# Kernel tuning notes

Measured on AMD Instinct MI355X. Metric: run time of the kernel, lower is better.

## Reference

```python
import jax, jax.numpy as jnp
import numpy as np

NUM_EXECUTORS = 50
NUM_DAG_FEATURES = 3
EMB_DAG = 16
EMB_GLOB = 16
HIDDEN = [64, 64, 32]
B = 60000            # number of jobs (one per env in the batched rollout)
NODES_PER_JOB = 10
NODE_FEAT = 5


def _init_mlp(key, dims):
    ws, bs = [], []
    for i in range(len(dims) - 1):
        key, k = jax.random.split(key)
        scale = 1.0 / np.sqrt(dims[i])
        ws.append(jax.random.uniform(k, (dims[i], dims[i + 1]), jnp.float32, -scale, scale))
        bs.append(jnp.zeros((dims[i + 1],), jnp.float32))
    return ws, bs


def setup_inputs() -> dict:
    rng = np.random.default_rng(0)
    n_nodes = B * NODES_PER_JOB
    # dag_batch.ptr: job i owns nodes [i*NODES_PER_JOB, (i+1)*NODES_PER_JOB)
    ptr = np.arange(B + 1, dtype=np.int64) * NODES_PER_JOB
    job_indices = rng.permutation(B).astype(np.int64)
    # ragged action counts per job (exec_mask is a prefix mask of length num_exec_acts[i])
    num_exec_acts = rng.integers(1, NUM_EXECUTORS + 1, size=B).astype(np.int64)
    n_sel = num_exec_acts[job_indices]
    T = int(n_sel.sum())
    # per-ragged-row executor index: concat([arange(n) for n in n_sel]), vectorized
    starts = np.cumsum(n_sel) - n_sel
    exec_act_idx = (np.arange(T, dtype=np.int64) - np.repeat(starts, n_sel)).astype(np.int64)

    key = jax.random.key(0)
    k_x, k_hd, k_hg, k_mlp = jax.random.split(key, 4)
    x = jax.random.normal(k_x, (n_nodes, NODE_FEAT), jnp.float32)
    h_dag = jax.random.normal(k_hd, (B, EMB_DAG), jnp.float32)
    h_glob = jax.random.normal(k_hg, (B, EMB_GLOB), jnp.float32)

    in_dim = NUM_DAG_FEATURES + EMB_DAG + EMB_GLOB + 1  # 36
    ws, bs = _init_mlp(k_mlp, [in_dim] + HIDDEN + [1])

    return {
        "x": x,
        "h_dag": h_dag,
        "h_glob": h_glob,
        "ptr": jnp.asarray(ptr),
        "job_indices": jnp.asarray(job_indices),
        "num_exec_acts": jnp.asarray(num_exec_acts),
        "exec_act_idx": jnp.asarray(exec_act_idx),
        "W1": ws[0], "b1": bs[0],
        "W2": ws[1], "b2": bs[1],
        "W3": ws[2], "b3": bs[2],
        "W4": ws[3], "b4": bs[3],
    }


def reference(x, h_dag, h_glob, ptr, job_indices, num_exec_acts, exec_act_idx,
              W1, b1, W2, b2, W3, b3, W4, b4):
    T = exec_act_idx.shape[0]                       # total ragged action rows (static)
    J = job_indices.shape[0]
    # masked gather: dag features at each dag's start node, then select jobs
    x_dag = x[ptr[:-1], :NUM_DAG_FEATURES][job_indices]        # [J, 3]
    h_dag_sel = h_dag[job_indices]                              # [J, 16]
    x_h_dag = jnp.concatenate([x_dag, h_dag_sel], axis=1)       # [J, 19]
    # variable repeat_interleave -> gather by repeated row index
    n_sel = num_exec_acts[job_indices]
    rpt = jnp.repeat(jnp.arange(J), n_sel, total_repeat_length=T)
    x_h_rpt = x_h_dag[rpt]                                      # [T, 19]
    h_glob_rpt = h_glob[rpt]                                    # [T, 16]
    # exec action feature: k / num_executors for the k-th valid executor
    exec_actions = (exec_act_idx.astype(x.dtype) / NUM_EXECUTORS)[:, None]  # [T, 1]
    h = jnp.concatenate([x_h_rpt, h_glob_rpt, exec_actions], axis=1)        # [T, 36]
    h = jax.nn.relu(h @ W1 + b1)
    h = jax.nn.relu(h @ W2 + b2)
    h = jax.nn.relu(h @ W3 + b3)
    scores = (h @ W4 + b4).squeeze(-1)                          # [T]
    return scores
```

## Files before the change

### kernel.cpp

```cpp
#include <hip/hip_runtime.h>

#define TPB 256

using half8  = __attribute__((ext_vector_type(8))) _Float16;
using fp16x2 = __attribute__((ext_vector_type(2))) __fp16;
using f32x4  = __attribute__((ext_vector_type(4))) float;

static __device__ __forceinline__ unsigned short h2u(_Float16 h) {
    union { _Float16 h; unsigned short u; } v; v.h = h; return v.u;
}
static __device__ __forceinline__ unsigned pkrtz(float a, float b) {
    fp16x2 h = __builtin_amdgcn_cvt_pkrtz(a, b);
    return __builtin_bit_cast(unsigned, h);
}
template <int CTRL>
static __device__ __forceinline__ float dppmov(float x) {
    return __int_as_float(__builtin_amdgcn_mov_dpp(__float_as_int(x), CTRL, 0xF, 0xF, true));
}
#define DPP_SWAP 0xB1

__global__ __launch_bounds__(TPB) void k_prep(const float* __restrict__ x,
                                              const float* __restrict__ h_dag,
                                              const float* __restrict__ h_glob,
                                              const int* __restrict__ ptr,
                                              const int* __restrict__ job_indices,
                                              const int* __restrict__ num_exec_acts,
                                              int J, unsigned int* __restrict__ feat,
                                              int* __restrict__ bsum)
{
    __shared__ int sc[TPB];
    int j = blockIdx.x * TPB + threadIdx.x;
    int v = 0;
    if (j < J) {
        int ji   = job_indices[j];
        v        = num_exec_acts[ji];
        int node = ptr[ji];
        float f[40];
        f[0] = x[node * 5 + 0];
        f[1] = x[node * 5 + 1];
        f[2] = x[node * 5 + 2];
#pragma unroll
        for (int c = 0; c < 16; c++) f[3 + c]  = h_dag[ji * 16 + c];
#pragma unroll
        for (int c = 0; c < 16; c++) f[19 + c] = h_glob[j * 16 + c];
#pragma unroll
        for (int c = 35; c < 40; c++) f[c] = 0.0f;
        unsigned int w[20];
#pragma unroll
        for (int k = 0; k < 20; k++)
            w[k] = (unsigned)h2u((_Float16)f[2 * k]) | ((unsigned)h2u((_Float16)f[2 * k + 1]) << 16);
        uint4* dst = (uint4*)(feat + (size_t)j * 20);
#pragma unroll
        for (int qq = 0; qq < 5; qq++)
            dst[qq] = make_uint4(w[4 * qq], w[4 * qq + 1], w[4 * qq + 2], w[4 * qq + 3]);
    }
    sc[threadIdx.x] = v;
    __syncthreads();
    for (int d = TPB / 2; d > 0; d >>= 1) {
        if (threadIdx.x < d) sc[threadIdx.x] += sc[threadIdx.x + d];
        __syncthreads();
    }
    if (threadIdx.x == 0) bsum[blockIdx.x] = sc[0];
}

__global__ __launch_bounds__(TPB) void k_scan_bsums(const int* __restrict__ bsum, int nb,
                                                    int* __restrict__ boff)
{
    __shared__ int sc[TPB];
    int v = (threadIdx.x < nb) ? bsum[threadIdx.x] : 0;
    sc[threadIdx.x] = v;
    __syncthreads();
    for (int d = 1; d < TPB; d <<= 1) {
        int add = (threadIdx.x >= d) ? sc[threadIdx.x - d] : 0;
        __syncthreads();
        sc[threadIdx.x] += add;
        __syncthreads();
    }
    if (threadIdx.x < nb) boff[threadIdx.x] = sc[threadIdx.x] - v;
}

__global__ __launch_bounds__(TPB) void k_starts_fill(const int* __restrict__ job_indices,
                                                     const int* __restrict__ num_exec_acts,
                                                     const int* __restrict__ boff,
                                                     int J, int* __restrict__ rpt)
{
    __shared__ int sc[TPB];
    int j = blockIdx.x * TPB + threadIdx.x;
    int v = (j < J) ? num_exec_acts[job_indices[j]] : 0;
    sc[threadIdx.x] = v;
    __syncthreads();
    for (int d = 1; d < TPB; d <<= 1) {
        int add = (threadIdx.x >= d) ? sc[threadIdx.x - d] : 0;
        __syncthreads();
        sc[threadIdx.x] += add;
        __syncthreads();
    }
    int start = boff[blockIdx.x] + sc[threadIdx.x] - v;
    if (j < J) {
        for (int k = 0; k < v; k++) rpt[start + k] = j;
    }
}

__global__ __launch_bounds__(TPB) void k_mlp_mfma(const unsigned int* __restrict__ feat,
                                                  const int* __restrict__ rpt,
                                                  const int* __restrict__ exec_act_idx,
                                                  const float* __restrict__ W1,
                                                  const float* __restrict__ b1,
                                                  const float* __restrict__ W2,
                                                  const float* __restrict__ b2,
                                                  const float* __restrict__ W3,
                                                  const float* __restrict__ b3,
                                                  const float* __restrict__ W4,
                                                  const float* __restrict__ b4,
                                                  float* __restrict__ out, int T, int numTiles)
{
    __shared__ __align__(16) char smem[4 * 8192];
    const int tid  = threadIdx.x;
    const int lane = tid & 63;
    const int wv   = tid >> 6;
    const int n    = lane & 15;
    const int q    = lane >> 4;
    char* slab0 = smem + wv * 8192;
    char* slab1 = slab0 + 4096;

    half8 bw1[4][2], bw2[4][2], bw3[2][2];
    float bb1[4], bb2[4], bb3[2];
#pragma unroll
    for (int nt = 0; nt < 4; nt++) {
        bb1[nt] = b1[nt * 16 + n];
        bb2[nt] = b2[nt * 16 + n];
#pragma unroll
        for (int s = 0; s < 2; s++) {
#pragma unroll
            for (int jj = 0; jj < 8; jj++) {
                int ks = s * 32 + q * 8 + jj;
                bw1[nt][s][jj] = (ks < 36) ? (_Float16)W1[ks * 64 + nt * 16 + n] : (_Float16)0.0f;
                bw2[nt][s][jj] = (_Float16)W2[ks * 64 + nt * 16 + n];
            }
        }
    }
#pragma unroll
    for (int nt = 0; nt < 2; nt++) {
        bb3[nt] = b3[nt * 16 + n];
#pragma unroll
        for (int s = 0; s < 2; s++) {
#pragma unroll
            for (int jj = 0; jj < 8; jj++) {
                int ks = s * 32 + q * 8 + jj;
                bw3[nt][s][jj] = (_Float16)W3[ks * 32 + nt * 16 + n];
            }
        }
    }
    const float w4a = W4[n];
    const float w4b = W4[16 + n];
    const float b4v = b4[0];
    const int   swr = (n >> 1) & 7;
    const int   odd = n & 1;

    for (int tile = blockIdx.x; tile < numTiles; tile += gridDim.x) {
        const int rowbase = tile * 128 + wv * 32;

        half8 a1[2][2];
#pragma unroll
        for (int mt = 0; mt < 2; mt++) {
            int  rt    = rowbase + 16 * mt + n;
            bool valid = rt < T;
            int  j     = valid ? rpt[rt] : 0;
            const uint4* fsrc = (const uint4*)(feat + (size_t)j * 20);
            uint4 g0 = fsrc[q];
            a1[mt][0] = __builtin_bit_cast(half8, g0);
            uint4 g1 = make_uint4(0, 0, 0, 0);
            if (q == 0) {
                g1 = fsrc[4];
                float fe = valid ? (float)exec_act_idx[rt] * 0.02f : 0.0f;
                g1.y = (g1.y & 0xffffu) | ((unsigned)h2u((_Float16)fe) << 16);
            }
            a1[mt][1] = __builtin_bit_cast(half8, g1);
        }

#pragma unroll
        for (int mt = 0; mt < 2; mt++) {
            f32x4 acc[4];
#pragma unroll
            for (int nt = 0; nt < 4; nt++) { f32x4 c; c[0]=c[1]=c[2]=c[3]=bb1[nt]; acc[nt]=c; }
#pragma unroll
            for (int s = 0; s < 2; s++) {
#pragma unroll
                for (int nt = 0; nt < 4; nt++)
                    acc[nt] = __builtin_amdgcn_mfma_f32_16x16x32_f16(a1[mt][s], bw1[nt][s], acc[nt], 0, 0, 0);
            }
            unsigned* sl = (unsigned*)slab0;
#pragma unroll
            for (int nt = 0; nt < 4; nt++) {
                float v0 = fmaxf(acc[nt][0], 0.0f), v1 = fmaxf(acc[nt][1], 0.0f);
                float v2 = fmaxf(acc[nt][2], 0.0f), v3 = fmaxf(acc[nt][3], 0.0f);
                float t0 = dppmov<DPP_SWAP>(v0), t1 = dppmov<DPP_SWAP>(v1);
                float t2 = dppmov<DPP_SWAP>(v2), t3 = dppmov<DPP_SWAP>(v3);
                unsigned u0 = pkrtz(odd ? t2 : v0, odd ? v2 : t0);
                unsigned u1 = pkrtz(odd ? t3 : v1, odd ? v3 : t1);
                int rowA = 16 * mt + 4 * q + (odd ? 2 : 0);
                int c    = 2 * nt + (n >> 3);
                int a0   = (rowA * 8 + (c ^ ((rowA >> 1) & 7))) * 4 + ((n >> 1) & 3);
                sl[a0] = u0; sl[a0 + 32] = u1;
            }
        }

#pragma unroll
        for (int mt = 0; mt < 2; mt++) {
            const int M0 = 16 * mt;
            f32x4 acc[4];
#pragma unroll
            for (int nt = 0; nt < 4; nt++) { f32x4 c; c[0]=c[1]=c[2]=c[3]=bb2[nt]; acc[nt]=c; }
#pragma unroll
            for (int s = 0; s < 2; s++) {
                half8 a = *(const half8*)(slab0 + ((M0 + n) * 8 + ((s * 4 + q) ^ swr)) * 16);
#pragma unroll
                for (int nt = 0; nt < 4; nt++)
                    acc[nt] = __builtin_amdgcn_mfma_f32_16x16x32_f16(a, bw2[nt][s], acc[nt], 0, 0, 0);
            }
            unsigned* sl = (unsigned*)slab1;
#pragma unroll
            for (int nt = 0; nt < 4; nt++) {
                float v0 = fmaxf(acc[nt][0], 0.0f), v1 = fmaxf(acc[nt][1], 0.0f);
                float v2 = fmaxf(acc[nt][2], 0.0f), v3 = fmaxf(acc[nt][3], 0.0f);
                float t0 = dppmov<DPP_SWAP>(v0), t1 = dppmov<DPP_SWAP>(v1);
                float t2 = dppmov<DPP_SWAP>(v2), t3 = dppmov<DPP_SWAP>(v3);
                unsigned u0 = pkrtz(odd ? t2 : v0, odd ? v2 : t0);
                unsigned u1 = pkrtz(odd ? t3 : v1, odd ? v3 : t1);
                int rowA = M0 + 4 * q + (odd ? 2 : 0);
                int c    = 2 * nt + (n >> 3);
                int a0   = (rowA * 8 + (c ^ ((rowA >> 1) & 7))) * 4 + ((n >> 1) & 3);
                sl[a0] = u0; sl[a0 + 32] = u1;
            }
        }

#pragma unroll
        for (int mt = 0; mt < 2; mt++) {
            const int M0 = 16 * mt;
            f32x4 acc[2];
#pragma unroll
            for (int nt = 0; nt < 2; nt++) { f32x4 c; c[0]=c[1]=c[2]=c[3]=bb3[nt]; acc[nt]=c; }
#pragma unroll
            for (int s = 0; s < 2; s++) {
                half8 a = *(const half8*)(slab1 + ((M0 + n) * 8 + ((s * 4 + q) ^ swr)) * 16);
#pragma unroll
                for (int nt = 0; nt < 2; nt++)
                    acc[nt] = __builtin_amdgcn_mfma_f32_16x16x32_f16(a, bw3[nt][s], acc[nt], 0, 0, 0);
            }
            f32x4 red;
#pragma unroll
            for (int r = 0; r < 4; r++)
                red[r] = fmaxf(acc[0][r], 0.0f) * w4a + fmaxf(acc[1][r], 0.0f) * w4b;
#pragma unroll
            for (int r = 0; r < 4; r++) {
                red[r] += dppmov<0x121>(red[r]);
                red[r] += dppmov<0x122>(red[r]);
                red[r] += dppmov<0x124>(red[r]);
                red[r] += dppmov<0x128>(red[r]);
            }
            int t = rowbase + M0 + q * 4 + n;
            float val = (n == 0) ? red[0] : (n == 1) ? red[1] : (n == 2) ? red[2] : red[3];
            if (n < 4 && t < T) out[t] = val + b4v;
        }
    }
}

extern "C" void kernel_launch(void* const* d_in, const int* in_sizes, int n_in,
                              void* d_out, int out_size, void* d_ws, size_t ws_size,
                              hipStream_t stream)
{
    const float* x             = (const float*)d_in[0];
    const float* h_dag         = (const float*)d_in[1];
    const float* h_glob        = (const float*)d_in[2];
    const int*   ptr           = (const int*)d_in[3];
    const int*   job_indices   = (const int*)d_in[4];
    const int*   num_exec_acts = (const int*)d_in[5];
    const int*   exec_act_idx  = (const int*)d_in[6];
    const float* W1 = (const float*)d_in[7];
    const float* b1 = (const float*)d_in[8];
    const float* W2 = (const float*)d_in[9];
    const float* b2 = (const float*)d_in[10];
    const float* W3 = (const float*)d_in[11];
    const float* b3 = (const float*)d_in[12];
    const float* W4 = (const float*)d_in[13];
    const float* b4 = (const float*)d_in[14];
    float* out = (float*)d_out;

    int J  = in_sizes[4];
    int T  = in_sizes[6];
    int nb = (J + TPB - 1) / TPB;

    char* wsp = (char*)d_ws;
    int* rpt = (int*)wsp;
    wsp += (((size_t)T * 4) + 255) / 256 * 256;
    int* bsum = (int*)wsp;
    wsp += (((size_t)nb * 4) + 255) / 256 * 256;
    int* boff = (int*)wsp;
    wsp += (((size_t)nb * 4) + 255) / 256 * 256;
    unsigned int* feat = (unsigned int*)wsp;

    k_prep<<<nb, TPB, 0, stream>>>(x, h_dag, h_glob, ptr, job_indices, num_exec_acts, J, feat, bsum);
    k_scan_bsums<<<1, TPB, 0, stream>>>(bsum, nb, boff);
    k_starts_fill<<<nb, TPB, 0, stream>>>(job_indices, num_exec_acts, boff, J, rpt);

    int numTiles = (T + 127) / 128;
    int grid = numTiles < 1024 ? numTiles : 1024;
    k_mlp_mfma<<<grid, TPB, 0, stream>>>(feat, rpt, exec_act_idx,
                                         W1, b1, W2, b2, W3, b3, W4, b4, out, T, numTiles);
}
```

Baseline: 184.0 us.

## Precompute MFMA weight fragments once and store per-job scan results in prep

The prep kernel now runs a full inclusive scan and writes each job's packed local offset and count, so the fill kernel no longer re-gathers num_exec_acts through job_indices or rescans. The single-block scan kernel also converts W1..W3, the biases and W4 into per-lane fp16 fragment layouts once. Each MLP block then loads these with a few vector loads instead of many strided scalar loads and conversions. The cost is extra workspace and a serial weight-prep step inside the one-block kernel.

```diff
diff --git a/kernel.cpp b/kernel.cpp
--- a/kernel.cpp
+++ b/kernel.cpp
@@ -26,7 +26,7 @@
                                               const int* __restrict__ job_indices,
                                               const int* __restrict__ num_exec_acts,
                                               int J, unsigned int* __restrict__ feat,
-                                              int* __restrict__ bsum)
+                                              int* __restrict__ bsum, int* __restrict__ jsv)
 {
     __shared__ int sc[TPB];
     int j = blockIdx.x * TPB + threadIdx.x;
@@ -56,15 +56,27 @@
     }
     sc[threadIdx.x] = v;
     __syncthreads();
-    for (int d = TPB / 2; d > 0; d >>= 1) {
-        if (threadIdx.x < d) sc[threadIdx.x] += sc[threadIdx.x + d];
+    for (int d = 1; d < TPB; d <<= 1) {
+        int add = (threadIdx.x >= d) ? sc[threadIdx.x - d] : 0;
         __syncthreads();
-    }
-    if (threadIdx.x == 0) bsum[blockIdx.x] = sc[0];
-}
-
-__global__ __launch_bounds__(TPB) void k_scan_bsums(const int* __restrict__ bsum, int nb,
-                                                    int* __restrict__ boff)
+        sc[threadIdx.x] += add;
+        __syncthreads();
+    }
+    if (j < J) jsv[j] = ((sc[threadIdx.x] - v) << 6) | v;
+    if (threadIdx.x == TPB - 1) bsum[blockIdx.x] = sc[TPB - 1];
+}
+
+__global__ __launch_bounds__(TPB) void k_scan_wprep(const int* __restrict__ bsum, int nb,
+                                                    int* __restrict__ boff,
+                                                    const float* __restrict__ W1,
+                                                    const float* __restrict__ b1,
+                                                    const float* __restrict__ W2,
+                                                    const float* __restrict__ b2,
+                                                    const float* __restrict__ W3,
+                                                    const float* __restrict__ b3,
+                                                    const float* __restrict__ W4,
+                                                    uint4* __restrict__ wfrag,
+                                                    float4* __restrict__ bfrag)
 {
     __shared__ int sc[TPB];
     int v = (threadIdx.x < nb) ? bsum[threadIdx.x] : 0;
@@ -77,40 +89,61 @@
         __syncthreads();
     }
     if (threadIdx.x < nb) boff[threadIdx.x] = sc[threadIdx.x] - v;
-}
-
-__global__ __launch_bounds__(TPB) void k_starts_fill(const int* __restrict__ job_indices,
-                                                     const int* __restrict__ num_exec_acts,
-                                                     const int* __restrict__ boff,
-                                                     int J, int* __restrict__ rpt)
-{
-    __shared__ int sc[TPB];
+
+    if (threadIdx.x < 64) {
+        int lane = threadIdx.x;
+        int n = lane & 15, q = lane >> 4;
+#pragma unroll
+        for (int nt = 0; nt < 4; nt++) {
+#pragma unroll
+            for (int s = 0; s < 2; s++) {
+                half8 w1f, w2f;
+#pragma unroll
+                for (int jj = 0; jj < 8; jj++) {
+                    int ks = s * 32 + q * 8 + jj;
+                    w1f[jj] = (ks < 36) ? (_Float16)W1[ks * 64 + nt * 16 + n] : (_Float16)0.0f;
+                    w2f[jj] = (_Float16)W2[ks * 64 + nt * 16 + n];
+                }
+                wfrag[(nt * 2 + s) * 64 + lane]     = __builtin_bit_cast(uint4, w1f);
+                wfrag[(8 + nt * 2 + s) * 64 + lane] = __builtin_bit_cast(uint4, w2f);
+            }
+        }
+#pragma unroll
+        for (int nt = 0; nt < 2; nt++) {
+#pragma unroll
+            for (int s = 0; s < 2; s++) {
+                half8 w3f;
+#pragma unroll
+                for (int jj = 0; jj < 8; jj++) {
+                    int ks = s * 32 + q * 8 + jj;
+                    w3f[jj] = (_Float16)W3[ks * 32 + nt * 16 + n];
+                }
+                wfrag[(16 + nt * 2 + s) * 64 + lane] = __builtin_bit_cast(uint4, w3f);
+            }
+        }
+        bfrag[0 * 64 + lane] = make_float4(b1[n], b1[16 + n], b1[32 + n], b1[48 + n]);
+        bfrag[1 * 64 + lane] = make_float4(b2[n], b2[16 + n], b2[32 + n], b2[48 + n]);
+        bfrag[2 * 64 + lane] = make_float4(b3[n], b3[16 + n], W4[n], W4[16 + n]);
+    }
+}
+
+__global__ __launch_bounds__(TPB) void k_fill(const int* __restrict__ jsv,
+                                              const int* __restrict__ boff,
+                                              int J, int* __restrict__ rpt)
+{
     int j = blockIdx.x * TPB + threadIdx.x;
-    int v = (j < J) ? num_exec_acts[job_indices[j]] : 0;
-    sc[threadIdx.x] = v;
-    __syncthreads();
-    for (int d = 1; d < TPB; d <<= 1) {
-        int add = (threadIdx.x >= d) ? sc[threadIdx.x - d] : 0;
-        __syncthreads();
-        sc[threadIdx.x] += add;
-        __syncthreads();
-    }
-    int start = boff[blockIdx.x] + sc[threadIdx.x] - v;
-    if (j < J) {
-        for (int k = 0; k < v; k++) rpt[start + k] = j;
-    }
+    if (j >= J) return;
+    int pv    = jsv[j];
+    int v     = pv & 63;
+    int start = boff[blockIdx.x] + (pv >> 6);
+    for (int k = 0; k < v; k++) rpt[start + k] = j;
 }
 
 __global__ __launch_bounds__(TPB) void k_mlp_mfma(const unsigned int* __restrict__ feat,
                                                   const int* __restrict__ rpt,
                                                   const int* __restrict__ exec_act_idx,
-                                                  const float* __restrict__ W1,
-                                                  const float* __restrict__ b1,
-                                                  const float* __restrict__ W2,
-                                                  const float* __restrict__ b2,
-                                                  const float* __restrict__ W3,
-                                                  const float* __restrict__ b3,
-                                                  const float* __restrict__ W4,
+                                                  const uint4* __restrict__ wfrag,
+                                                  const float4* __restrict__ bfrag,
                                                   const float* __restrict__ b4,
                                                   float* __restrict__ out, int T, int numTiles)
 {
@@ -124,35 +157,26 @@
     char* slab1 = slab0 + 4096;
 
     half8 bw1[4][2], bw2[4][2], bw3[2][2];
-    float bb1[4], bb2[4], bb3[2];
-#pragma unroll
-    for (int nt = 0; nt < 4; nt++) {
-        bb1[nt] = b1[nt * 16 + n];
-        bb2[nt] = b2[nt * 16 + n];
+#pragma unroll
+    for (int nt = 0; nt < 4; nt++)
 #pragma unroll
         for (int s = 0; s < 2; s++) {
-#pragma unroll
-            for (int jj = 0; jj < 8; jj++) {
-                int ks = s * 32 + q * 8 + jj;
-                bw1[nt][s][jj] = (ks < 36) ? (_Float16)W1[ks * 64 + nt * 16 + n] : (_Float16)0.0f;
-                bw2[nt][s][jj] = (_Float16)W2[ks * 64 + nt * 16 + n];
-            }
-        }
-    }
-#pragma unroll
-    for (int nt = 0; nt < 2; nt++) {
-        bb3[nt] = b3[nt * 16 + n];
-#pragma unroll
-        for (int s = 0; s < 2; s++) {
-#pragma unroll
-            for (int jj = 0; jj < 8; jj++) {
-                int ks = s * 32 + q * 8 + jj;
-                bw3[nt][s][jj] = (_Float16)W3[ks * 32 + nt * 16 + n];
-            }
-        }
-    }
-    const float w4a = W4[n];
-    const float w4b = W4[16 + n];
+            bw1[nt][s] = __builtin_bit_cast(half8, wfrag[(nt * 2 + s) * 64 + lane]);
+            bw2[nt][s] = __builtin_bit_cast(half8, wfrag[(8 + nt * 2 + s) * 64 + lane]);
+        }
+#pragma unroll
+    for (int nt = 0; nt < 2; nt++)
+#pragma unroll
+        for (int s = 0; s < 2; s++)
+            bw3[nt][s] = __builtin_bit_cast(half8, wfrag[(16 + nt * 2 + s) * 64 + lane]);
+
+    float4 bf1 = bfrag[0 * 64 + lane];
+    float4 bf2 = bfrag[1 * 64 + lane];
+    float4 bf3 = bfrag[2 * 64 + lane];
+    float bb1[4] = {bf1.x, bf1.y, bf1.z, bf1.w};
+    float bb2[4] = {bf2.x, bf2.y, bf2.z, bf2.w};
+    float bb3[2] = {bf3.x, bf3.y};
+    const float w4a = bf3.z, w4b = bf3.w;
     const float b4v = b4[0];
     const int   swr = (n >> 1) & 7;
     const int   odd = n & 1;
@@ -297,14 +321,22 @@
     wsp += (((size_t)nb * 4) + 255) / 256 * 256;
     int* boff = (int*)wsp;
     wsp += (((size_t)nb * 4) + 255) / 256 * 256;
+    int* jsv = (int*)wsp;
+    wsp += (((size_t)J * 4) + 255) / 256 * 256;
+    uint4* wfrag = (uint4*)wsp;
+    wsp += 20 * 64 * 16;
+    float4* bfrag = (float4*)wsp;
+    wsp += 3 * 64 * 16;
     unsigned int* feat = (unsigned int*)wsp;
 
-    k_prep<<<nb, TPB, 0, stream>>>(x, h_dag, h_glob, ptr, job_indices, num_exec_acts, J, feat, bsum);
-    k_scan_bsums<<<1, TPB, 0, stream>>>(bsum, nb, boff);
-    k_starts_fill<<<nb, TPB, 0, stream>>>(job_indices, num_exec_acts, boff, J, rpt);
+    k_prep<<<nb, TPB, 0, stream>>>(x, h_dag, h_glob, ptr, job_indices, num_exec_acts,
+                                   J, feat, bsum, jsv);
+    k_scan_wprep<<<1, TPB, 0, stream>>>(bsum, nb, boff, W1, b1, W2, b2, W3, b3, W4,
+                                        wfrag, bfrag);
+    k_fill<<<nb, TPB, 0, stream>>>(jsv, boff, J, rpt);
 
     int numTiles = (T + 127) / 128;
     int grid = numTiles < 1024 ? numTiles : 1024;
-    k_mlp_mfma<<<grid, TPB, 0, stream>>>(feat, rpt, exec_act_idx,
-                                         W1, b1, W2, b2, W3, b3, W4, b4, out, T, numTiles);
-}
+    k_mlp_mfma<<<grid, TPB, 0, stream>>>(feat, rpt, exec_act_idx, wfrag, bfrag, b4,
+                                         out, T, numTiles);
+}
```

Result: no change. 181.0 us (-1.6%).
